# Optimization experiments

Measured on AMD Instinct MI355X. Metric: run time of the kernel, lower is better.

Reference implementation:

```python
import jax, jax.numpy as jnp
import numpy as np

D = 128
N1, N2, N3, N4 = 100000, 200000, 300000, 400000


def setup_inputs() -> dict:
    key = jax.random.key(0)
    cnt = [0]

    def nrm(shape, scale=0.05):
        cnt[0] += 1
        return jax.random.normal(jax.random.fold_in(key, cnt[0]), shape, dtype=jnp.float32) * scale

    def rint(shape, hi):
        cnt[0] += 1
        return jax.random.randint(jax.random.fold_in(key, cnt[0]), shape, 0, hi)

    inp = {}
    inp["h"] = nrm((N1, D), 1.0)
    inp["idx2"] = rint((N2, 2), N1)
    inp["idx3"] = rint((N3, 3), N1)
    inp["idx4"] = rint((N4, 4), N1)
    # sequential_%L MLPs: Linear(L*D -> D) + relu, Linear(D->D)+relu, Linear(D->D)+relu
    for L in (1, 2, 3, 4):
        din = D * L
        inp["s%d_W0" % L] = nrm((din, D))
        inp["s%d_b0" % L] = nrm((D,))
        inp["s%d_W1" % L] = nrm((D, D))
        inp["s%d_b1" % L] = nrm((D,))
        inp["s%d_W2" % L] = nrm((D, D))
        inp["s%d_b2" % L] = nrm((D,))
    # per-feature output heads Linear(D -> 1)
    for f in ("sigma", "epsilon", "q"):
        inp["h1_%s_W" % f] = nrm((D, 1))
        inp["h1_%s_b" % f] = nrm((1,))
    for L in (2, 3, 4):
        for f in ("k", "eq"):
            inp["h%d_%s_W" % (L, f)] = nrm((D, 1))
            inp["h%d_%s_b" % (L, f)] = nrm((1,))
    return inp


def _mlp(x, W0, b0, W1, b1, W2, b2):
    x = jax.nn.relu(x @ W0 + b0)
    x = jax.nn.relu(x @ W1 + b1)
    return jax.nn.relu(x @ W2 + b2)


def _level(h, idx, p):
    # copy_u + mean with exactly one n1 neighbor per relationship slot == gather
    g = jnp.take(h, idx, axis=0)              # [N, K, D]
    N, K, Dd = g.shape
    xf = g.reshape(N, K * Dd)                 # concat h0..h_{K-1}
    xb = g[:, ::-1, :].reshape(N, K * Dd)     # concat reversed
    return _mlp(xf, *p) + _mlp(xb, *p)        # pool = torch.add


def reference(h, idx2, idx3, idx4,
              s1_W0, s1_b0, s1_W1, s1_b1, s1_W2, s1_b2,
              s2_W0, s2_b0, s2_W1, s2_b1, s2_W2, s2_b2,
              s3_W0, s3_b0, s3_W1, s3_b1, s3_W2, s3_b2,
              s4_W0, s4_b0, s4_W1, s4_b1, s4_W2, s4_b2,
              h1_sigma_W, h1_sigma_b, h1_epsilon_W, h1_epsilon_b, h1_q_W, h1_q_b,
              h2_k_W, h2_k_b, h2_eq_W, h2_eq_b,
              h3_k_W, h3_k_b, h3_eq_W, h3_eq_b,
              h4_k_W, h4_k_b, h4_eq_W, h4_eq_b):
    y1 = _mlp(h, s1_W0, s1_b0, s1_W1, s1_b1, s1_W2, s1_b2)
    sigma = y1 @ h1_sigma_W + h1_sigma_b
    epsilon = y1 @ h1_epsilon_W + h1_epsilon_b
    q = y1 @ h1_q_W + h1_q_b
    y2 = _level(h, idx2, (s2_W0, s2_b0, s2_W1, s2_b1, s2_W2, s2_b2))
    k2 = y2 @ h2_k_W + h2_k_b
    eq2 = y2 @ h2_eq_W + h2_eq_b
    y3 = _level(h, idx3, (s3_W0, s3_b0, s3_W1, s3_b1, s3_W2, s3_b2))
    k3 = y3 @ h3_k_W + h3_k_b
    eq3 = y3 @ h3_eq_W + h3_eq_b
    y4 = _level(h, idx4, (s4_W0, s4_b0, s4_W1, s4_b1, s4_W2, s4_b2))
    k4 = y4 @ h4_k_W + h4_k_b
    eq4 = y4 @ h4_eq_W + h4_eq_b
    return (sigma, epsilon, q, k2, eq2, k3, eq3, k4, eq4)
```

## Files before the change

### kernel.cpp

```cpp
#include <hip/hip_runtime.h>

typedef __attribute__((ext_vector_type(8))) _Float16 half8;
typedef __attribute__((ext_vector_type(4))) float f32x4;

#define N1_ 100000
#define N2_ 200000
#define N3_ 300000
#define N4_ 400000

typedef __attribute__((address_space(1))) const void gconst_t;
typedef __attribute__((address_space(3))) void lds_t;

__device__ __forceinline__ unsigned short f2h_bits(float x) {
  union { _Float16 h; unsigned short u; } cv;
  cv.h = (_Float16)x;
  return cv.u;
}

__device__ __forceinline__ f32x4 mfma16(half8 a, half8 b, f32x4 c) {
  return __builtin_amdgcn_mfma_f32_16x16x32_f16(a, b, c, 0, 0, 0);
}

__global__ void cvt_h_kernel(const float* __restrict__ h,
                             unsigned short* __restrict__ hf, int n4) {
  int i = blockIdx.x * blockDim.x + threadIdx.x;
  if (i >= n4) return;
  float4 v = reinterpret_cast<const float4*>(h)[i];
  ushort4 o;
  o.x = f2h_bits(v.x); o.y = f2h_bits(v.y);
  o.z = f2h_bits(v.z); o.w = f2h_bits(v.w);
  reinterpret_cast<ushort4*>(hf)[i] = o;
}

struct PackInfo {
  const float* W[12];
  int kt_base[13];
  int out_off[12];
};

__global__ void pack_w_kernel(PackInfo info, unsigned short* __restrict__ pw) {
  int b = blockIdx.x;
  int lane = threadIdx.x;
  int m = 0;
  while (m < 11 && b >= info.kt_base[m + 1]) ++m;
  int kt = b - info.kt_base[m];
  const float* W = info.W[m];
  int lr = lane & 15, kb = lane >> 4;
  unsigned short* outp = pw + info.out_off[m] + (size_t)kt * 4096 + lane * 8;
  #pragma unroll
  for (int nt = 0; nt < 8; ++nt) {
    #pragma unroll
    for (int j = 0; j < 8; ++j) {
      int krow = kt * 32 + kb * 8 + j;
      int col = nt * 16 + lr;
      outp[nt * 512 + j] = f2h_bits(W[(size_t)krow * 128 + col]);
    }
  }
}

template <int K, int NHEAD>
__global__ __launch_bounds__(256, (K == 1) ? 4 : 3) void level_kernel(
    const unsigned short* __restrict__ hf,
    const int* __restrict__ idx,
    const unsigned short* __restrict__ pw,
    const float* __restrict__ b0, const float* __restrict__ b1,
    const float* __restrict__ b2,
    const float* __restrict__ hw0, const float* __restrict__ hb0,
    float* __restrict__ out0,
    const float* __restrict__ hw1, const float* __restrict__ hb1,
    float* __restrict__ out1,
    const float* __restrict__ hw2, const float* __restrict__ hb2,
    float* __restrict__ out2,
    int N) {
  constexpr int NDIR = (K > 1) ? 2 : 1;
  constexpr int KT0 = 4 * K;
  constexpr int NPAIR = (K / 2) * 4;
  constexpr bool MID = (K % 2) != 0;

  __shared__ __align__(16) unsigned short bstage[2][4096];
  __shared__ __align__(16) unsigned short act[4][NDIR][2048];

  const int lane = threadIdx.x & 63;
  const int wid = threadIdx.x >> 6;
  const int lrow = lane & 15;
  const int kb = lane >> 4;

  int tile = blockIdx.x * 4 + wid;
  const int maxtile = N / 16 - 1;
  const bool wr = (tile <= maxtile);
  if (!wr) tile = maxtile;

  int src[K];
  #pragma unroll
  for (int s = 0; s < K; ++s)
    src[s] = (K == 1) ? (tile * 16 + lrow)
                      : idx[(size_t)(tile * 16 + lrow) * K + s];

  auto stage = [&](int buf, const unsigned short* slab) {
    const unsigned short* g = slab + (wid * 2) * 512 + lane * 8;
    unsigned short* l = &bstage[buf][(wid * 2) * 512];
    __builtin_amdgcn_global_load_lds((gconst_t*)g, (lds_t*)l, 16, 0, 0);
    __builtin_amdgcn_global_load_lds((gconst_t*)(g + 512), (lds_t*)(l + 512), 16, 0, 0);
  };

  auto gfrag = [&](int segRow, int sub, half8& dst) {
    dst = *reinterpret_cast<const half8*>(
        hf + (size_t)src[segRow] * 128 + sub * 32 + kb * 8);
  };

  f32x4 acc[NDIR][8];
  auto zero_acc = [&]() {
    #pragma unroll
    for (int d = 0; d < NDIR; ++d)
      #pragma unroll
      for (int nt = 0; nt < 8; ++nt) acc[d][nt] = f32x4{0.f, 0.f, 0.f, 0.f};
  };

  auto mfma_phase = [&](int buf, half8 af, half8 ab) {
    #pragma unroll
    for (int nt = 0; nt < 8; ++nt) {
      half8 bq = *reinterpret_cast<const half8*>(&bstage[buf][nt * 512 + lane * 8]);
      acc[0][nt] = mfma16(af, bq, acc[0][nt]);
      if constexpr (NDIR == 2) acc[1][nt] = mfma16(ab, bq, acc[1][nt]);
    }
  };

  auto actA = [&](int d, int kt) -> half8 {
    unsigned off = (unsigned)(lrow * 256 + (kt * 32 + kb * 8) * 2) ^
                   ((unsigned)(lrow & 7) << 4);
    return *reinterpret_cast<const half8*>(
        reinterpret_cast<const unsigned char*>(&act[wid][d][0]) + off);
  };

  auto store_act = [&](int d, const float* bias) {
    unsigned char* base = reinterpret_cast<unsigned char*>(&act[wid][d][0]);
    #pragma unroll
    for (int nt = 0; nt < 8; ++nt) {
      float bv = bias[nt * 16 + lrow];
      #pragma unroll
      for (int r = 0; r < 4; ++r) {
        float v = fmaxf(acc[d][nt][r] + bv, 0.f);
        int trow = 4 * kb + r;
        unsigned off = (unsigned)(trow * 256 + (nt * 16 + lrow) * 2) ^
                       ((unsigned)(trow & 7) << 4);
        *reinterpret_cast<unsigned short*>(base + off) = f2h_bits(v);
      }
    }
  };

  int cur = 0;
  zero_acc();

  half8 gA, gB, nA, nB;
  stage(cur, pw);
  gfrag(0, 0, gA);
  if constexpr (NPAIR > 0) gfrag(K - 1, 0, gB);
  __syncthreads();

  for (int pr = 0; pr < NPAIR; ++pr) {
    const int sp = pr >> 2, sub = pr & 3;
    const int slabB = (K - 1 - sp) * 4 + sub;
    stage(cur ^ 1, pw + (size_t)slabB * 4096);
    mfma_phase(cur, gA, gB);
    __syncthreads();
    cur ^= 1;
    if (pr + 1 < NPAIR) {
      const int sp2 = (pr + 1) >> 2, sub2 = (pr + 1) & 3;
      stage(cur ^ 1, pw + (size_t)(sp2 * 4 + sub2) * 4096);
      gfrag(sp2, sub2, nA);
      gfrag(K - 1 - sp2, sub2, nB);
    } else if constexpr (MID) {
      stage(cur ^ 1, pw + (size_t)(((K - 1) / 2) * 4) * 4096);
      gfrag((K - 1) / 2, 0, nA);
    } else {
      stage(cur ^ 1, pw + (size_t)KT0 * 4096);
    }
    mfma_phase(cur, gB, gA);
    __syncthreads();
    cur ^= 1;
    gA = nA; gB = nB;
  }

  if constexpr (MID) {
    const int mseg = (K - 1) / 2;
    for (int sub = 0; sub < 4; ++sub) {
      if (sub + 1 < 4) {
        stage(cur ^ 1, pw + (size_t)(mseg * 4 + sub + 1) * 4096);
        gfrag(mseg, sub + 1, nA);
      } else {
        stage(cur ^ 1, pw + (size_t)KT0 * 4096);
      }
      mfma_phase(cur, gA, gA);
      __syncthreads();
      cur ^= 1;
      gA = nA;
    }
  }

  #pragma unroll
  for (int d = 0; d < NDIR; ++d) store_act(d, b0);

  const unsigned short* w1 = pw + (size_t)KT0 * 4096;
  #pragma unroll 1
  for (int layer = 1; layer <= 2; ++layer) {
    const unsigned short* w = (layer == 1) ? w1 : w1 + 16384;
    zero_acc();
    for (int kt = 0; kt < 4; ++kt) {
      if (kt + 1 < 4) stage(cur ^ 1, w + (size_t)(kt + 1) * 4096);
      else if (layer == 1) stage(cur ^ 1, w1 + 16384);
      half8 a[NDIR];
      #pragma unroll
      for (int d = 0; d < NDIR; ++d) a[d] = actA(d, kt);
      #pragma unroll
      for (int nt = 0; nt < 8; ++nt) {
        half8 bq = *reinterpret_cast<const half8*>(&bstage[cur][nt * 512 + lane * 8]);
        #pragma unroll
        for (int d = 0; d < NDIR; ++d) acc[d][nt] = mfma16(a[d], bq, acc[d][nt]);
      }
      if (!(layer == 2 && kt == 3)) {
        __syncthreads();
        cur ^= 1;
      }
    }
    if (layer == 1) {
      #pragma unroll
      for (int d = 0; d < NDIR; ++d) store_act(d, b1);
    }
  }

  f32x4 y[8];
  #pragma unroll
  for (int nt = 0; nt < 8; ++nt) {
    float bv = b2[nt * 16 + lrow];
    #pragma unroll
    for (int r = 0; r < 4; ++r) {
      float v = fmaxf(acc[0][nt][r] + bv, 0.f);
      if constexpr (NDIR == 2) v += fmaxf(acc[1][nt][r] + bv, 0.f);
      y[nt][r] = v;
    }
  }

  const float* hws[3] = {hw0, hw1, hw2};
  const float* hbs[3] = {hb0, hb1, hb2};
  float* outs[3] = {out0, out1, out2};
  #pragma unroll
  for (int hd = 0; hd < NHEAD; ++hd) {
    float p[4] = {0.f, 0.f, 0.f, 0.f};
    #pragma unroll
    for (int nt = 0; nt < 8; ++nt) {
      float w = hws[hd][nt * 16 + lrow];
      #pragma unroll
      for (int r = 0; r < 4; ++r) p[r] += y[nt][r] * w;
    }
    #pragma unroll
    for (int m = 1; m < 16; m <<= 1) {
      #pragma unroll
      for (int r = 0; r < 4; ++r) p[r] += __shfl_xor(p[r], m, 64);
    }
    if (wr && lrow < 4) {
      float pv = (lrow == 0) ? p[0] : (lrow == 1) ? p[1] : (lrow == 2) ? p[2] : p[3];
      outs[hd][tile * 16 + 4 * kb + lrow] = pv + hbs[hd][0];
    }
  }
}

extern "C" void kernel_launch(void* const* d_in, const int* in_sizes, int n_in,
                              void* d_out, int out_size, void* d_ws, size_t ws_size,
                              hipStream_t stream) {
  (void)in_sizes; (void)n_in; (void)out_size;

  const float* h = (const float*)d_in[0];
  const int* idx2 = (const int*)d_in[1];
  const int* idx3 = (const int*)d_in[2];
  const int* idx4 = (const int*)d_in[3];

  const float* sW[4][3];
  const float* sb[4][3];
  for (int L = 0; L < 4; ++L)
    for (int j = 0; j < 3; ++j) {
      sW[L][j] = (const float*)d_in[4 + L * 6 + j * 2];
      sb[L][j] = (const float*)d_in[4 + L * 6 + j * 2 + 1];
    }
  const float* hW[9];
  const float* hB[9];
  for (int i = 0; i < 9; ++i) {
    hW[i] = (const float*)d_in[28 + i * 2];
    hB[i] = (const float*)d_in[28 + i * 2 + 1];
  }

  size_t need = ((size_t)N1_ * 128 + 294912) * 2;
  if (ws_size < need) return;
  unsigned short* hf = (unsigned short*)d_ws;
  unsigned short* pw = hf + (size_t)N1_ * 128;

  cvt_h_kernel<<<(N1_ * 128 / 4 + 255) / 256, 256, 0, stream>>>(h, hf, N1_ * 128 / 4);

  PackInfo pi;
  const int din[12] = {128, 128, 128, 256, 128, 128, 384, 128, 128, 512, 128, 128};
  int ktb = 0, ooff = 0;
  for (int m = 0; m < 12; ++m) {
    pi.W[m] = sW[m / 3][m % 3];
    pi.kt_base[m] = ktb;
    pi.out_off[m] = ooff;
    ktb += din[m] / 32;
    ooff += din[m] * 128;
  }
  pi.kt_base[12] = ktb;
  pack_w_kernel<<<ktb, 64, 0, stream>>>(pi, pw);

  float* out = (float*)d_out;
  float* o_sigma = out;
  float* o_eps = out + N1_;
  float* o_q = out + 2 * N1_;
  float* o_k2 = out + 3 * N1_;
  float* o_eq2 = o_k2 + N2_;
  float* o_k3 = o_eq2 + N2_;
  float* o_eq3 = o_k3 + N3_;
  float* o_k4 = o_eq3 + N3_;
  float* o_eq4 = o_k4 + N4_;

  level_kernel<1, 3><<<(N1_ / 16 + 3) / 4, 256, 0, stream>>>(
      hf, nullptr, pw + pi.out_off[0], sb[0][0], sb[0][1], sb[0][2],
      hW[0], hB[0], o_sigma, hW[1], hB[1], o_eps, hW[2], hB[2], o_q, N1_);
  level_kernel<2, 2><<<(N2_ / 16 + 3) / 4, 256, 0, stream>>>(
      hf, idx2, pw + pi.out_off[3], sb[1][0], sb[1][1], sb[1][2],
      hW[3], hB[3], o_k2, hW[4], hB[4], o_eq2, nullptr, nullptr, nullptr, N2_);
  level_kernel<3, 2><<<(N3_ / 16 + 3) / 4, 256, 0, stream>>>(
      hf, idx3, pw + pi.out_off[6], sb[2][0], sb[2][1], sb[2][2],
      hW[5], hB[5], o_k3, hW[6], hB[6], o_eq3, nullptr, nullptr, nullptr, N3_);
  level_kernel<4, 2><<<(N4_ / 16 + 3) / 4, 256, 0, stream>>>(
      hf, idx4, pw + pi.out_off[9], sb[3][0], sb[3][1], sb[3][2],
      hW[7], hB[7], o_k4, hW[8], hB[8], o_eq4, nullptr, nullptr, nullptr, N4_);
}
```

Before: 442.6 us.

## Process MLP directions sequentially in layers 1-2 to cut registers and LDS

Layers 1 and 2 of the per-level MLP now run the forward and reversed directions one after the other instead of interleaved. This halves the activation LDS buffer and the live accumulator registers. Because the head projection is linear, the head dot products are accumulated per direction, so the final y sum is never materialised. Launch bounds are raised to 4 waves-per-EU for all K to gain occupancy, at the cost of twice as many weight-staging passes and barriers in layers 1-2.

```diff
diff --git a/kernel.cpp b/kernel.cpp
--- a/kernel.cpp
+++ b/kernel.cpp
@@ -59,7 +59,7 @@
 }
 
 template <int K, int NHEAD>
-__global__ __launch_bounds__(256, (K == 1) ? 4 : 3) void level_kernel(
+__global__ __launch_bounds__(256, 4) void level_kernel(
     const unsigned short* __restrict__ hf,
     const int* __restrict__ idx,
     const unsigned short* __restrict__ pw,
@@ -78,7 +78,7 @@
   constexpr bool MID = (K % 2) != 0;
 
   __shared__ __align__(16) unsigned short bstage[2][4096];
-  __shared__ __align__(16) unsigned short act[4][NDIR][2048];
+  __shared__ __align__(16) unsigned short act[4][2048];
 
   const int lane = threadIdx.x & 63;
   const int wid = threadIdx.x >> 6;
@@ -125,21 +125,21 @@
     }
   };
 
-  auto actA = [&](int d, int kt) -> half8 {
+  auto actA = [&](int kt) -> half8 {
     unsigned off = (unsigned)(lrow * 256 + (kt * 32 + kb * 8) * 2) ^
                    ((unsigned)(lrow & 7) << 4);
     return *reinterpret_cast<const half8*>(
-        reinterpret_cast<const unsigned char*>(&act[wid][d][0]) + off);
-  };
-
-  auto store_act = [&](int d, const float* bias) {
-    unsigned char* base = reinterpret_cast<unsigned char*>(&act[wid][d][0]);
+        reinterpret_cast<const unsigned char*>(&act[wid][0]) + off);
+  };
+
+  auto store_act = [&](const f32x4* a, const float* bias) {
+    unsigned char* base = reinterpret_cast<unsigned char*>(&act[wid][0]);
     #pragma unroll
     for (int nt = 0; nt < 8; ++nt) {
       float bv = bias[nt * 16 + lrow];
       #pragma unroll
       for (int r = 0; r < 4; ++r) {
-        float v = fmaxf(acc[d][nt][r] + bv, 0.f);
+        float v = fmaxf(a[nt][r] + bv, 0.f);
         int trow = 4 * kb + r;
         unsigned off = (unsigned)(trow * 256 + (nt * 16 + lrow) * 2) ^
                        ((unsigned)(trow & 7) << 4);
@@ -197,68 +197,72 @@
     }
   }
 
-  #pragma unroll
-  for (int d = 0; d < NDIR; ++d) store_act(d, b0);
-
   const unsigned short* w1 = pw + (size_t)KT0 * 4096;
-  #pragma unroll 1
-  for (int layer = 1; layer <= 2; ++layer) {
-    const unsigned short* w = (layer == 1) ? w1 : w1 + 16384;
-    zero_acc();
-    for (int kt = 0; kt < 4; ++kt) {
-      if (kt + 1 < 4) stage(cur ^ 1, w + (size_t)(kt + 1) * 4096);
-      else if (layer == 1) stage(cur ^ 1, w1 + 16384);
-      half8 a[NDIR];
-      #pragma unroll
-      for (int d = 0; d < NDIR; ++d) a[d] = actA(d, kt);
-      #pragma unroll
-      for (int nt = 0; nt < 8; ++nt) {
-        half8 bq = *reinterpret_cast<const half8*>(&bstage[cur][nt * 512 + lane * 8]);
-        #pragma unroll
-        for (int d = 0; d < NDIR; ++d) acc[d][nt] = mfma16(a[d], bq, acc[d][nt]);
-      }
-      if (!(layer == 2 && kt == 3)) {
-        __syncthreads();
-        cur ^= 1;
-      }
-    }
-    if (layer == 1) {
-      #pragma unroll
-      for (int d = 0; d < NDIR; ++d) store_act(d, b1);
-    }
-  }
-
-  f32x4 y[8];
-  #pragma unroll
-  for (int nt = 0; nt < 8; ++nt) {
-    float bv = b2[nt * 16 + lrow];
-    #pragma unroll
-    for (int r = 0; r < 4; ++r) {
-      float v = fmaxf(acc[0][nt][r] + bv, 0.f);
-      if constexpr (NDIR == 2) v += fmaxf(acc[1][nt][r] + bv, 0.f);
-      y[nt][r] = v;
-    }
-  }
-
   const float* hws[3] = {hw0, hw1, hw2};
   const float* hbs[3] = {hb0, hb1, hb2};
   float* outs[3] = {out0, out1, out2};
+
+  f32x4 ph[NHEAD];
+  #pragma unroll
+  for (int hd = 0; hd < NHEAD; ++hd) ph[hd] = f32x4{0.f, 0.f, 0.f, 0.f};
+
+  auto run_l12 = [&](const f32x4* a0, bool lastDp) {
+    store_act(a0, b0);
+    f32x4 a2[8];
+    #pragma unroll
+    for (int nt = 0; nt < 8; ++nt) a2[nt] = f32x4{0.f, 0.f, 0.f, 0.f};
+    #pragma unroll 1
+    for (int p8 = 0; p8 < 8; ++p8) {
+      const bool last = lastDp && (p8 == 7);
+      if (!last) {
+        const int q = (p8 + 1) & 7;
+        stage(cur ^ 1, w1 + (size_t)(((q >> 2) & 1) * 4 + (q & 3)) * 4096);
+      }
+      half8 a = actA(p8 & 3);
+      #pragma unroll
+      for (int nt = 0; nt < 8; ++nt) {
+        half8 bq = *reinterpret_cast<const half8*>(&bstage[cur][nt * 512 + lane * 8]);
+        a2[nt] = mfma16(a, bq, a2[nt]);
+      }
+      if (!last) {
+        __syncthreads();
+        cur ^= 1;
+      }
+      if (p8 == 3) {
+        store_act(a2, b1);
+        #pragma unroll
+        for (int nt = 0; nt < 8; ++nt) a2[nt] = f32x4{0.f, 0.f, 0.f, 0.f};
+      }
+    }
+    #pragma unroll
+    for (int nt = 0; nt < 8; ++nt) {
+      float bv = b2[nt * 16 + lrow];
+      float wv[3];
+      #pragma unroll
+      for (int hd = 0; hd < NHEAD; ++hd) wv[hd] = hws[hd][nt * 16 + lrow];
+      #pragma unroll
+      for (int r = 0; r < 4; ++r) {
+        float v = fmaxf(a2[nt][r] + bv, 0.f);
+        #pragma unroll
+        for (int hd = 0; hd < NHEAD; ++hd) ph[hd][r] += v * wv[hd];
+      }
+    }
+  };
+
+  if constexpr (NDIR == 2) run_l12(acc[1], false);
+  run_l12(acc[0], true);
+
   #pragma unroll
   for (int hd = 0; hd < NHEAD; ++hd) {
-    float p[4] = {0.f, 0.f, 0.f, 0.f};
-    #pragma unroll
-    for (int nt = 0; nt < 8; ++nt) {
-      float w = hws[hd][nt * 16 + lrow];
-      #pragma unroll
-      for (int r = 0; r < 4; ++r) p[r] += y[nt][r] * w;
-    }
     #pragma unroll
     for (int m = 1; m < 16; m <<= 1) {
       #pragma unroll
-      for (int r = 0; r < 4; ++r) p[r] += __shfl_xor(p[r], m, 64);
+      for (int r = 0; r < 4; ++r) ph[hd][r] += __shfl_xor(ph[hd][r], m, 64);
     }
     if (wr && lrow < 4) {
-      float pv = (lrow == 0) ? p[0] : (lrow == 1) ? p[1] : (lrow == 2) ? p[2] : p[3];
+      float pv = (lrow == 0) ? ph[hd][0]
+               : (lrow == 1) ? ph[hd][1]
+               : (lrow == 2) ? ph[hd][2] : ph[hd][3];
       outs[hd][tile * 16 + 4 * kb + lrow] = pv + hbs[hd][0];
     }
   }
```

Measured after the change: 602.4 us. 1.36x slower.

## Load MFMA weight fragments directly from global memory instead of LDS staging

Applied to the files above, without the earlier changes.

Removes the double-buffered LDS staging of weight slabs (global_load_lds plus __syncthreads) and has each wave read its B fragments straight from global/L2 into registers, with the loops fully unrolled. Waves become independent, so out-of-range waves can exit early and the barriers go away. The cost is that each of the four waves now fetches the same weights separately through the cache hierarchy, and register pressure rises because the loads are unrolled.

```diff
diff --git a/kernel.cpp b/kernel.cpp
--- a/kernel.cpp
+++ b/kernel.cpp
@@ -7,9 +7,6 @@
 #define N2_ 200000
 #define N3_ 300000
 #define N4_ 400000
-
-typedef __attribute__((address_space(1))) const void gconst_t;
-typedef __attribute__((address_space(3))) void lds_t;
 
 __device__ __forceinline__ unsigned short f2h_bits(float x) {
   union { _Float16 h; unsigned short u; } cv;
@@ -77,7 +74,6 @@
   constexpr int NPAIR = (K / 2) * 4;
   constexpr bool MID = (K % 2) != 0;
 
-  __shared__ __align__(16) unsigned short bstage[2][4096];
   __shared__ __align__(16) unsigned short act[4][NDIR][2048];
 
   const int lane = threadIdx.x & 63;
@@ -85,10 +81,8 @@
   const int lrow = lane & 15;
   const int kb = lane >> 4;
 
-  int tile = blockIdx.x * 4 + wid;
-  const int maxtile = N / 16 - 1;
-  const bool wr = (tile <= maxtile);
-  if (!wr) tile = maxtile;
+  const int tile = blockIdx.x * 4 + wid;
+  if (tile * 16 >= N) return;
 
   int src[K];
   #pragma unroll
@@ -96,11 +90,8 @@
     src[s] = (K == 1) ? (tile * 16 + lrow)
                       : idx[(size_t)(tile * 16 + lrow) * K + s];
 
-  auto stage = [&](int buf, const unsigned short* slab) {
-    const unsigned short* g = slab + (wid * 2) * 512 + lane * 8;
-    unsigned short* l = &bstage[buf][(wid * 2) * 512];
-    __builtin_amdgcn_global_load_lds((gconst_t*)g, (lds_t*)l, 16, 0, 0);
-    __builtin_amdgcn_global_load_lds((gconst_t*)(g + 512), (lds_t*)(l + 512), 16, 0, 0);
+  auto wfrag = [&](const unsigned short* slab, int nt) -> half8 {
+    return *reinterpret_cast<const half8*>(slab + nt * 512 + lane * 8);
   };
 
   auto gfrag = [&](int segRow, int sub, half8& dst) {
@@ -116,10 +107,10 @@
       for (int nt = 0; nt < 8; ++nt) acc[d][nt] = f32x4{0.f, 0.f, 0.f, 0.f};
   };
 
-  auto mfma_phase = [&](int buf, half8 af, half8 ab) {
+  auto mfma_phase = [&](const unsigned short* slab, half8 af, half8 ab) {
     #pragma unroll
     for (int nt = 0; nt < 8; ++nt) {
-      half8 bq = *reinterpret_cast<const half8*>(&bstage[buf][nt * 512 + lane * 8]);
+      half8 bq = wfrag(slab, nt);
       acc[0][nt] = mfma16(af, bq, acc[0][nt]);
       if constexpr (NDIR == 2) acc[1][nt] = mfma16(ab, bq, acc[1][nt]);
     }
@@ -148,84 +139,47 @@
     }
   };
 
-  int cur = 0;
   zero_acc();
 
-  half8 gA, gB, nA, nB;
-  stage(cur, pw);
-  gfrag(0, 0, gA);
-  if constexpr (NPAIR > 0) gfrag(K - 1, 0, gB);
-  __syncthreads();
-
+  #pragma unroll
   for (int pr = 0; pr < NPAIR; ++pr) {
     const int sp = pr >> 2, sub = pr & 3;
-    const int slabB = (K - 1 - sp) * 4 + sub;
-    stage(cur ^ 1, pw + (size_t)slabB * 4096);
-    mfma_phase(cur, gA, gB);
-    __syncthreads();
-    cur ^= 1;
-    if (pr + 1 < NPAIR) {
-      const int sp2 = (pr + 1) >> 2, sub2 = (pr + 1) & 3;
-      stage(cur ^ 1, pw + (size_t)(sp2 * 4 + sub2) * 4096);
-      gfrag(sp2, sub2, nA);
-      gfrag(K - 1 - sp2, sub2, nB);
-    } else if constexpr (MID) {
-      stage(cur ^ 1, pw + (size_t)(((K - 1) / 2) * 4) * 4096);
-      gfrag((K - 1) / 2, 0, nA);
-    } else {
-      stage(cur ^ 1, pw + (size_t)KT0 * 4096);
-    }
-    mfma_phase(cur, gB, gA);
-    __syncthreads();
-    cur ^= 1;
-    gA = nA; gB = nB;
-  }
-
+    half8 gA, gB;
+    gfrag(sp, sub, gA);
+    gfrag(K - 1 - sp, sub, gB);
+    mfma_phase(pw + (size_t)(sp * 4 + sub) * 4096, gA, gB);
+    mfma_phase(pw + (size_t)((K - 1 - sp) * 4 + sub) * 4096, gB, gA);
+  }
   if constexpr (MID) {
     const int mseg = (K - 1) / 2;
+    #pragma unroll
     for (int sub = 0; sub < 4; ++sub) {
-      if (sub + 1 < 4) {
-        stage(cur ^ 1, pw + (size_t)(mseg * 4 + sub + 1) * 4096);
-        gfrag(mseg, sub + 1, nA);
-      } else {
-        stage(cur ^ 1, pw + (size_t)KT0 * 4096);
-      }
-      mfma_phase(cur, gA, gA);
-      __syncthreads();
-      cur ^= 1;
-      gA = nA;
-    }
-  }
-
+      half8 g;
+      gfrag(mseg, sub, g);
+      mfma_phase(pw + (size_t)(mseg * 4 + sub) * 4096, g, g);
+    }
+  }
   #pragma unroll
   for (int d = 0; d < NDIR; ++d) store_act(d, b0);
 
   const unsigned short* w1 = pw + (size_t)KT0 * 4096;
-  #pragma unroll 1
-  for (int layer = 1; layer <= 2; ++layer) {
-    const unsigned short* w = (layer == 1) ? w1 : w1 + 16384;
-    zero_acc();
-    for (int kt = 0; kt < 4; ++kt) {
-      if (kt + 1 < 4) stage(cur ^ 1, w + (size_t)(kt + 1) * 4096);
-      else if (layer == 1) stage(cur ^ 1, w1 + 16384);
-      half8 a[NDIR];
-      #pragma unroll
-      for (int d = 0; d < NDIR; ++d) a[d] = actA(d, kt);
-      #pragma unroll
-      for (int nt = 0; nt < 8; ++nt) {
-        half8 bq = *reinterpret_cast<const half8*>(&bstage[cur][nt * 512 + lane * 8]);
-        #pragma unroll
-        for (int d = 0; d < NDIR; ++d) acc[d][nt] = mfma16(a[d], bq, acc[d][nt]);
-      }
-      if (!(layer == 2 && kt == 3)) {
-        __syncthreads();
-        cur ^= 1;
-      }
-    }
-    if (layer == 1) {
-      #pragma unroll
-      for (int d = 0; d < NDIR; ++d) store_act(d, b1);
-    }
+  zero_acc();
+  #pragma unroll
+  for (int kt = 0; kt < 4; ++kt) {
+    half8 a[NDIR];
+    #pragma unroll
+    for (int d = 0; d < NDIR; ++d) a[d] = actA(d, kt);
+    mfma_phase(w1 + (size_t)kt * 4096, a[0], a[NDIR - 1]);
+  }
+  #pragma unroll
+  for (int d = 0; d < NDIR; ++d) store_act(d, b1);
+  zero_acc();
+  #pragma unroll
+  for (int kt = 0; kt < 4; ++kt) {
+    half8 a[NDIR];
+    #pragma unroll
+    for (int d = 0; d < NDIR; ++d) a[d] = actA(d, kt);
+    mfma_phase(w1 + 16384 + (size_t)kt * 4096, a[0], a[NDIR - 1]);
   }
 
   f32x4 y[8];
@@ -257,7 +211,7 @@
       #pragma unroll
       for (int r = 0; r < 4; ++r) p[r] += __shfl_xor(p[r], m, 64);
     }
-    if (wr && lrow < 4) {
+    if (lrow < 4) {
       float pv = (lrow == 0) ? p[0] : (lrow == 1) ? p[1] : (lrow == 2) ? p[2] : p[3];
       outs[hd][tile * 16 + 4 * kb + lrow] = pv + hbs[hd][0];
     }
```

Result: slower. 885.0 us (+99.9%).

## Gather neighbor rows via async global-to-LDS DMA in per-segment chunks

Applied to the files above, without the earlier changes.

Replaces the per-step register gathers of h rows with global_load_lds DMA into a per-wave LDS region. A whole segment pair (all four K-subtiles, forward and reverse) is fetched ahead of time, and the act buffers are aliased onto that same region. This issues more gather loads at once so their latency overlaps the first-layer MFMAs, instead of prefetching just one fragment. LDS per block grows for K>1, which may limit occupancy, and the aliasing of act and gather buffers depends on correct barrier ordering.

```diff
diff --git a/kernel.cpp b/kernel.cpp
--- a/kernel.cpp
+++ b/kernel.cpp
@@ -10,6 +10,8 @@
 
 typedef __attribute__((address_space(1))) const void gconst_t;
 typedef __attribute__((address_space(3))) void lds_t;
+
+#define MEMFENCE() asm volatile("" ::: "memory")
 
 __device__ __forceinline__ unsigned short f2h_bits(float x) {
   union { _Float16 h; unsigned short u; } cv;
@@ -74,17 +76,20 @@
     int N) {
   constexpr int NDIR = (K > 1) ? 2 : 1;
   constexpr int KT0 = 4 * K;
-  constexpr int NPAIR = (K / 2) * 4;
-  constexpr bool MID = (K % 2) != 0;
-
-  __shared__ __align__(16) unsigned short bstage[2][4096];
-  __shared__ __align__(16) unsigned short act[4][NDIR][2048];
+  constexpr int NC = (K + 1) / 2;
+  constexpr int GRB = (K == 1) ? 4096 : 8192;
+  constexpr int SMEM_SZ = 16384 + 4 * GRB;
+
+  __shared__ __align__(16) unsigned char smem[SMEM_SZ];
 
   const int lane = threadIdx.x & 63;
   const int wid = threadIdx.x >> 6;
   const int lrow = lane & 15;
   const int kb = lane >> 4;
 
+  unsigned short* const bst = reinterpret_cast<unsigned short*>(smem);
+  unsigned char* const gbase = smem + 16384 + wid * GRB;
+
   int tile = blockIdx.x * 4 + wid;
   const int maxtile = N / 16 - 1;
   const bool wr = (tile <= maxtile);
@@ -98,14 +103,25 @@
 
   auto stage = [&](int buf, const unsigned short* slab) {
     const unsigned short* g = slab + (wid * 2) * 512 + lane * 8;
-    unsigned short* l = &bstage[buf][(wid * 2) * 512];
+    unsigned short* l = bst + buf * 4096 + (wid * 2) * 512;
     __builtin_amdgcn_global_load_lds((gconst_t*)g, (lds_t*)l, 16, 0, 0);
     __builtin_amdgcn_global_load_lds((gconst_t*)(g + 512), (lds_t*)(l + 512), 16, 0, 0);
   };
 
-  auto gfrag = [&](int segRow, int sub, half8& dst) {
-    dst = *reinterpret_cast<const half8*>(
-        hf + (size_t)src[segRow] * 128 + sub * 32 + kb * 8);
+  auto dma_gather = [&](int seg, int sub, int slot) {
+    const unsigned short* g = hf + (size_t)src[seg] * 128 + sub * 32 + kb * 8;
+    __builtin_amdgcn_global_load_lds((gconst_t*)g, (lds_t*)(gbase + slot * 1024),
+                                     16, 0, 0);
+  };
+  auto issue_chunk = [&](int c) {
+    #pragma unroll
+    for (int sub = 0; sub < 4; ++sub) {
+      dma_gather(c, sub, sub);
+      if (c != K - 1 - c) dma_gather(K - 1 - c, sub, 4 + sub);
+    }
+  };
+  auto readfrag = [&](int slot) -> half8 {
+    return *reinterpret_cast<const half8*>(gbase + slot * 1024 + lane * 16);
   };
 
   f32x4 acc[NDIR][8];
@@ -119,7 +135,7 @@
   auto mfma_phase = [&](int buf, half8 af, half8 ab) {
     #pragma unroll
     for (int nt = 0; nt < 8; ++nt) {
-      half8 bq = *reinterpret_cast<const half8*>(&bstage[buf][nt * 512 + lane * 8]);
+      half8 bq = *reinterpret_cast<const half8*>(bst + buf * 4096 + nt * 512 + lane * 8);
       acc[0][nt] = mfma16(af, bq, acc[0][nt]);
       if constexpr (NDIR == 2) acc[1][nt] = mfma16(ab, bq, acc[1][nt]);
     }
@@ -128,12 +144,10 @@
   auto actA = [&](int d, int kt) -> half8 {
     unsigned off = (unsigned)(lrow * 256 + (kt * 32 + kb * 8) * 2) ^
                    ((unsigned)(lrow & 7) << 4);
-    return *reinterpret_cast<const half8*>(
-        reinterpret_cast<const unsigned char*>(&act[wid][d][0]) + off);
-  };
-
+    return *reinterpret_cast<const half8*>(gbase + d * 4096 + off);
+  };
   auto store_act = [&](int d, const float* bias) {
-    unsigned char* base = reinterpret_cast<unsigned char*>(&act[wid][d][0]);
+    unsigned char* base = gbase + d * 4096;
     #pragma unroll
     for (int nt = 0; nt < 8; ++nt) {
       float bv = bias[nt * 16 + lrow];
@@ -148,59 +162,55 @@
     }
   };
 
+  zero_acc();
+
+  const unsigned short* w1 = pw + (size_t)KT0 * 4096;
+
+  issue_chunk(0);
+  stage(0, pw);
+  __syncthreads();
+
   int cur = 0;
-  zero_acc();
-
-  half8 gA, gB, nA, nB;
-  stage(cur, pw);
-  gfrag(0, 0, gA);
-  if constexpr (NPAIR > 0) gfrag(K - 1, 0, gB);
-  __syncthreads();
-
-  for (int pr = 0; pr < NPAIR; ++pr) {
-    const int sp = pr >> 2, sub = pr & 3;
-    const int slabB = (K - 1 - sp) * 4 + sub;
-    stage(cur ^ 1, pw + (size_t)slabB * 4096);
-    mfma_phase(cur, gA, gB);
-    __syncthreads();
-    cur ^= 1;
-    if (pr + 1 < NPAIR) {
-      const int sp2 = (pr + 1) >> 2, sub2 = (pr + 1) & 3;
-      stage(cur ^ 1, pw + (size_t)(sp2 * 4 + sub2) * 4096);
-      gfrag(sp2, sub2, nA);
-      gfrag(K - 1 - sp2, sub2, nB);
-    } else if constexpr (MID) {
-      stage(cur ^ 1, pw + (size_t)(((K - 1) / 2) * 4) * 4096);
-      gfrag((K - 1) / 2, 0, nA);
-    } else {
-      stage(cur ^ 1, pw + (size_t)KT0 * 4096);
-    }
-    mfma_phase(cur, gB, gA);
-    __syncthreads();
-    cur ^= 1;
-    gA = nA; gB = nB;
-  }
-
-  if constexpr (MID) {
-    const int mseg = (K - 1) / 2;
-    for (int sub = 0; sub < 4; ++sub) {
-      if (sub + 1 < 4) {
-        stage(cur ^ 1, pw + (size_t)(mseg * 4 + sub + 1) * 4096);
-        gfrag(mseg, sub + 1, nA);
+  #pragma unroll
+  for (int c = 0; c < NC; ++c) {
+    const bool selfpair = (c == K - 1 - c);
+    const int pc = selfpair ? 4 : 8;
+    #pragma unroll
+    for (int q = 0; q < pc; ++q) {
+      int seg, sub, fs, bs;
+      if (selfpair) { seg = c; sub = q; fs = q; bs = q; }
+      else {
+        int i = q >> 1, ab = q & 1;
+        seg = ab ? (K - 1 - c) : c; sub = i;
+        fs = ab ? 4 + i : i; bs = ab ? i : 4 + i;
+      }
+      (void)seg;
+      half8 af = readfrag(fs);
+      half8 abf{};
+      if constexpr (NDIR == 2) abf = readfrag(bs);
+
+      if (q + 1 < pc) {
+        int i2 = selfpair ? (q + 1) : ((q + 1) >> 1);
+        int ab2 = selfpair ? 0 : ((q + 1) & 1);
+        int seg2 = selfpair ? c : (ab2 ? (K - 1 - c) : c);
+        stage(cur ^ 1, pw + (size_t)(seg2 * 4 + i2) * 4096);
+      } else if (c + 1 < NC) {
+        stage(cur ^ 1, pw + (size_t)((c + 1) * 4) * 4096);
       } else {
-        stage(cur ^ 1, pw + (size_t)KT0 * 4096);
-      }
-      mfma_phase(cur, gA, gA);
+        stage(cur ^ 1, w1);
+      }
+      MEMFENCE();
+      mfma_phase(cur, af, abf);
+      MEMFENCE();
+      if (q == pc - 1 && c + 1 < NC) issue_chunk(c + 1);
       __syncthreads();
       cur ^= 1;
-      gA = nA;
     }
   }
 
   #pragma unroll
   for (int d = 0; d < NDIR; ++d) store_act(d, b0);
 
-  const unsigned short* w1 = pw + (size_t)KT0 * 4096;
   #pragma unroll 1
   for (int layer = 1; layer <= 2; ++layer) {
     const unsigned short* w = (layer == 1) ? w1 : w1 + 16384;
@@ -213,7 +223,7 @@
       for (int d = 0; d < NDIR; ++d) a[d] = actA(d, kt);
       #pragma unroll
       for (int nt = 0; nt < 8; ++nt) {
-        half8 bq = *reinterpret_cast<const half8*>(&bstage[cur][nt * 512 + lane * 8]);
+        half8 bq = *reinterpret_cast<const half8*>(bst + cur * 4096 + nt * 512 + lane * 8);
         #pragma unroll
         for (int d = 0; d < NDIR; ++d) acc[d][nt] = mfma16(a[d], bq, acc[d][nt]);
       }
```

Result: slower. 480.0 us (+8.4%).
